# Performance work log

Measured on AMD Instinct MI355X. Metric: run time of the kernel, lower is better.

## Reference

```python
import jax, jax.numpy as jnp
import numpy as np

N_NODES = 50000
N_EDGES = 800000
N_FEAT = 128
HIDDEN = 128
N_CLASSES = 10
N_GRAPHS = 100


def setup_inputs() -> dict:
    key = jax.random.key(0)
    ks = jax.random.split(key, 16)
    x = jax.random.normal(ks[0], (N_NODES, N_FEAT), dtype=jnp.float32)
    edge_index = jax.random.randint(ks[1], (2, N_EDGES), 0, N_NODES, dtype=jnp.int64)
    batch = jnp.sort(jax.random.randint(ks[2], (N_NODES,), 0, N_GRAPHS, dtype=jnp.int64))

    def glorot(k, fi, fo):
        s = jnp.sqrt(6.0 / (fi + fo)).astype(jnp.float32)
        return jax.random.uniform(k, (fi, fo), jnp.float32, -s, s)

    return {
        "x": x,
        "edge_index": edge_index,
        "batch": batch,
        "W1": glorot(ks[3], N_FEAT, HIDDEN),
        "b1": jnp.zeros((HIDDEN,), jnp.float32),
        "W2": glorot(ks[4], HIDDEN, HIDDEN),
        "b2": jnp.zeros((HIDDEN,), jnp.float32),
        "W3": glorot(ks[5], HIDDEN, HIDDEN // 2),
        "b3": jnp.zeros((HIDDEN // 2,), jnp.float32),
        "Wf1": glorot(ks[6], HIDDEN // 2, 32),
        "bf1": jnp.zeros((32,), jnp.float32),
        "Wf2": glorot(ks[7], 32, N_CLASSES),
        "bf2": jnp.zeros((N_CLASSES,), jnp.float32),
    }


def _gcn_conv(x, row, col, norm, W, b, n_nodes):
    # GCNConv: x' = D^{-1/2}(A+I)D^{-1/2} (x W) + b
    h = x @ W                                            # [N, out]
    msg = h[row] * norm[:, None]                         # gather + scale per edge
    out = jax.ops.segment_sum(msg, col, num_segments=n_nodes)  # scatter-add to targets
    return out + b


def reference(x, edge_index, batch, W1, b1, W2, b2, W3, b3, Wf1, bf1, Wf2, bf2):
    n = x.shape[0]
    # add self-loops (PyG GCNConv default)
    loop = jnp.arange(n, dtype=edge_index.dtype)
    row = jnp.concatenate([edge_index[0], loop])
    col = jnp.concatenate([edge_index[1], loop])
    # symmetric normalization from in-degree at targets (edge_weight = 1)
    deg = jax.ops.segment_sum(jnp.ones_like(col, x.dtype), col, num_segments=n)
    dinv = jnp.where(deg > 0, jax.lax.rsqrt(deg), 0.0)
    norm = dinv[row] * dinv[col]                         # [E + N]

    h = jax.nn.relu(_gcn_conv(x, row, col, norm, W1, b1, n))
    h = jax.nn.relu(_gcn_conv(h, row, col, norm, W2, b2, n))
    h = jax.nn.relu(_gcn_conv(h, row, col, norm, W3, b3, n))

    # global_mean_pool over graphs
    sums = jax.ops.segment_sum(h, batch, num_segments=N_GRAPHS)
    cnts = jax.ops.segment_sum(jnp.ones((n,), h.dtype), batch, num_segments=N_GRAPHS)
    pooled = sums / jnp.maximum(cnts, 1.0)[:, None]      # [G, hidden//2]

    h = jax.nn.relu(pooled @ Wf1 + bf1)
    logits = h @ Wf2 + bf2                               # [G, num_classes]
    return logits
```

## Files before the change

kernel.cpp:

```cpp
#include <hip/hip_runtime.h>
#include <hip/hip_fp16.h>


#define NGRAPH 100
#define CAP 64

typedef _Float16 f16x8 __attribute__((ext_vector_type(8)));
typedef float f32x4 __attribute__((ext_vector_type(4)));
typedef float fx2 __attribute__((ext_vector_type(2)));


__global__ __launch_bounds__(256) void prep_all(const float* __restrict__ W1,
                                                const float* __restrict__ W2,
                                                const float* __restrict__ W3,
                                                __half* __restrict__ Wt1,
                                                __half* __restrict__ Wt2,
                                                __half* __restrict__ Wt3,
                                                int* __restrict__ cnt,
                                                float* __restrict__ pooled, int n) {
    const int idx = blockIdx.x * 256 + threadIdx.x;
    if (idx < 16384) {
        int nn = idx >> 7, k = idx & 127;
        Wt1[idx] = __float2half(W1[k * 128 + nn]);
    } else if (idx < 32768) {
        int j = idx - 16384;
        int nn = j >> 7, k = j & 127;
        Wt2[j] = __float2half(W2[k * 128 + nn]);
    } else if (idx < 40960) {
        int j = idx - 32768;
        int nn = j >> 7, k = j & 127;
        Wt3[j] = __float2half(W3[k * 64 + nn]);
    }
    if (idx < n) cnt[idx] = 0;
    if (idx < NGRAPH * 64) pooled[idx] = 0.0f;
}


__global__ void fill_bucket(const int* __restrict__ row, const int* __restrict__ col,
                            int* __restrict__ cnt, int* __restrict__ bucket,
                            int E, int colsPerGroup) {
    const int g  = blockIdx.x & 7;
    const int gb = blockIdx.x >> 3;
    const int nb = gridDim.x >> 3;
    const int lo = g * colsPerGroup, hi = lo + colsPerGroup;
    for (int e = gb * 256 + threadIdx.x; e < E; e += nb * 256) {
        int c = col[e];
        if (c >= lo && c < hi) {
            int pos = atomicAdd(&cnt[c], 1);
            bucket[c * CAP + pos] = row[e];
        }
    }
}


template <int OUT, bool F16IN>
__global__ __launch_bounds__(256) void gemm_mfma(const void* __restrict__ Xv,
                                                 const __half* __restrict__ Wt,
                                                 const float* __restrict__ bias_in,
                                                 const int* __restrict__ cnt,
                                                 __half* __restrict__ Yh, int n) {
    __shared__ _Float16 Xs[64 * 128];
    __shared__ _Float16 Ws[OUT * 128];
    __shared__ float bs[128];

    const float*  Xf = (const float*)Xv;
    const __half* Xh = (const __half*)Xv;

    const int t = threadIdx.x;
    if (t < 128) bs[t] = (bias_in != nullptr) ? bias_in[t] : 0.0f;
    __syncthreads();

    const int row0 = blockIdx.x * 64;
    const bool do_relu = (bias_in != nullptr);

    for (int c = t; c < 64 * 16; c += 256) {
        const int r = c >> 4, q = c & 15;
        const int gr = row0 + r;
        float vals[8];
        #pragma unroll
        for (int i = 0; i < 8; ++i) vals[i] = 0.0f;
        if (gr < n) {
            if (F16IN) {
                f16x8 hv = *(const f16x8*)&Xh[(size_t)gr * 128 + q * 8];
                #pragma unroll
                for (int i = 0; i < 8; ++i) vals[i] = (float)hv[i];
            } else {
                float4 va = *(const float4*)&Xf[(size_t)gr * 128 + q * 8];
                float4 vb = *(const float4*)&Xf[(size_t)gr * 128 + q * 8 + 4];
                vals[0] = va.x; vals[1] = va.y; vals[2] = va.z; vals[3] = va.w;
                vals[4] = vb.x; vals[5] = vb.y; vals[6] = vb.z; vals[7] = vb.w;
            }
        }
        if (do_relu) {
            const int k = q * 8;
            #pragma unroll
            for (int i = 0; i < 8; ++i) vals[i] = fmaxf(vals[i] + bs[k + i], 0.f);
        }
        f16x8 hv;
        #pragma unroll
        for (int i = 0; i < 8; ++i) hv[i] = (_Float16)vals[i];
        *(f16x8*)&Xs[(size_t)((r << 4) + (q ^ (r & 15))) * 8] = hv;
    }
    for (int c = t; c < OUT * 16; c += 256) {
        const int nn = c >> 4, q = c & 15;
        f16x8 w = *(const f16x8*)&Wt[nn * 128 + q * 8];
        *(f16x8*)&Ws[(size_t)((nn << 4) + (q ^ (nn & 15))) * 8] = w;
    }
    __syncthreads();

    constexpr int NT = OUT / 16;
    const int lane = t & 63, wave = t >> 6;
    const int m = lane & 15, quad = lane >> 4;

    f32x4 acc[NT];
    #pragma unroll
    for (int i = 0; i < NT; ++i) acc[i] = (f32x4){0.f, 0.f, 0.f, 0.f};

    #pragma unroll
    for (int s = 0; s < 4; ++s) {
        const int qa = s * 4 + quad;
        f16x8 a = *(const f16x8*)&Xs[(size_t)(((wave * 16 + m) << 4) + (qa ^ m)) * 8];
        #pragma unroll
        for (int tt = 0; tt < NT; ++tt) {
            f16x8 b = *(const f16x8*)&Ws[(size_t)(((tt * 16 + m) << 4) + (qa ^ m)) * 8];
            acc[tt] = __builtin_amdgcn_mfma_f32_16x16x32_f16(a, b, acc[tt], 0, 0, 0);
        }
    }

    #pragma unroll
    for (int i = 0; i < 4; ++i) {
        const int gr = row0 + wave * 16 + quad * 4 + i;
        if (gr < n) {
            const float dw = 1.0f / sqrtf((float)(cnt[gr] + 1));
            #pragma unroll
            for (int tt = 0; tt < NT; ++tt)
                Yh[(size_t)gr * OUT + tt * 16 + m] = __float2half(acc[tt][i] * dw);
        }
    }
}


template <int F>
__global__ void gather_kernel(const __half* __restrict__ hs, const int* __restrict__ cnt,
                              const int* __restrict__ bucket,
                              __half* __restrict__ outh, int n) {
    const int lane = threadIdx.x & 63;
    const int c = (blockIdx.x * blockDim.x + threadIdx.x) >> 6;
    if (c >= n) return;
    const int deg = cnt[c];
    const int beg = c * CAP;
    const int end = beg + deg;
    const int last = end - 1;
    const float w = 1.0f / sqrtf((float)(deg + 1));
    const float2* hq = (const float2*)hs;

    auto cvt = [](float2 raw) {
        __half2 ha = *(__half2*)&raw.x;
        __half2 hb = *(__half2*)&raw.y;
        float2 fa = __half22float2(ha);
        float2 fb = __half22float2(hb);
        return make_float4(fa.x, fa.y, fb.x, fb.y);
    };

    if (F == 128) {
        const int half = lane >> 5;
        const int l    = lane & 31;
        float4 acc = make_float4(0.f, 0.f, 0.f, 0.f);
        if (half == 0) acc = cvt(hq[(size_t)c * 32 + l]);
        const int chunks = (deg + 7) >> 3;
        int j = beg + half;
        for (int t = 0; t < chunks; ++t, j += 8) {
            const int j0 = j, j1 = j + 2, j2 = j + 4, j3 = j + 6;
            const int s0 = __builtin_nontemporal_load(&bucket[min(j0, last)]);
            const int s1 = __builtin_nontemporal_load(&bucket[min(j1, last)]);
            const int s2 = __builtin_nontemporal_load(&bucket[min(j2, last)]);
            const int s3 = __builtin_nontemporal_load(&bucket[min(j3, last)]);
            const float m0 = (j0 < end) ? 1.f : 0.f;
            const float m1 = (j1 < end) ? 1.f : 0.f;
            const float m2 = (j2 < end) ? 1.f : 0.f;
            const float m3 = (j3 < end) ? 1.f : 0.f;
            float4 v0 = cvt(hq[(size_t)s0 * 32 + l]);
            float4 v1 = cvt(hq[(size_t)s1 * 32 + l]);
            float4 v2 = cvt(hq[(size_t)s2 * 32 + l]);
            float4 v3 = cvt(hq[(size_t)s3 * 32 + l]);
            acc.x += m0 * v0.x + m1 * v1.x + m2 * v2.x + m3 * v3.x;
            acc.y += m0 * v0.y + m1 * v1.y + m2 * v2.y + m3 * v3.y;
            acc.z += m0 * v0.z + m1 * v1.z + m2 * v2.z + m3 * v3.z;
            acc.w += m0 * v0.w + m1 * v1.w + m2 * v2.w + m3 * v3.w;
        }
        acc.x += __shfl(acc.x, lane ^ 32);
        acc.y += __shfl(acc.y, lane ^ 32);
        acc.z += __shfl(acc.z, lane ^ 32);
        acc.w += __shfl(acc.w, lane ^ 32);
        if (half == 0) {
            __half2 h0 = __float22half2_rn(make_float2(w * acc.x, w * acc.y));
            __half2 h1 = __float22half2_rn(make_float2(w * acc.z, w * acc.w));
            fx2 o;
            o[0] = *(float*)&h0;
            o[1] = *(float*)&h1;
            __builtin_nontemporal_store(o, (fx2*)&outh[(size_t)c * 128 + l * 4]);
        }
    }
}


__global__ __launch_bounds__(256) void fused_gpool(const __half* __restrict__ hs,
                                                   const int* __restrict__ cnt,
                                                   const int* __restrict__ bucket,
                                                   const float* __restrict__ b3,
                                                   const int* __restrict__ batch,
                                                   float* __restrict__ pooled, int n) {
    const int lane  = threadIdx.x & 63;
    const int half  = lane >> 5;
    const int li    = lane & 31;
    const int wave  = (blockIdx.x * blockDim.x + threadIdx.x) >> 6;
    const int nwav  = (gridDim.x * blockDim.x) >> 6;
    const int chunk = (n + nwav - 1) / nwav;
    const int beg = wave * chunk;
    const int end = min(beg + chunk, n);
    if (beg >= end) return;
    const unsigned* h2 = (const unsigned*)hs;

    auto cvt2 = [](unsigned raw) { return __half22float2(*(__half2*)&raw); };

    const float bias0 = b3[li * 2], bias1 = b3[li * 2 + 1];
    int curg = batch[beg];
    float2 acc = make_float2(0.f, 0.f);
    for (int i = beg; i < end; ++i) {
        int g = batch[i];
        if (g != curg) {
            if (half == 0) {
                atomicAdd(&pooled[curg * 64 + li * 2],     acc.x);
                atomicAdd(&pooled[curg * 64 + li * 2 + 1], acc.y);
            }
            acc = make_float2(0.f, 0.f); curg = g;
        }
        const int deg = cnt[i];
        const float dv = 1.0f / sqrtf((float)(deg + 1));
        float2 sv = make_float2(0.f, 0.f);
        if (half == 0) sv = cvt2(h2[(size_t)i * 32 + li]);
        const int eb = i * CAP, ee = eb + deg;
        const int lastj = ee - 1;
        const int chks = (deg + 15) >> 4;
        int j = eb + half;
        for (int t = 0; t < chks; ++t, j += 16) {
            const int j0 = j,      j1 = j + 2,  j2 = j + 4,  j3 = j + 6;
            const int j4 = j + 8,  j5 = j + 10, j6 = j + 12, j7 = j + 14;
            const int a0 = __builtin_nontemporal_load(&bucket[min(j0, lastj)]);
            const int a1 = __builtin_nontemporal_load(&bucket[min(j1, lastj)]);
            const int a2 = __builtin_nontemporal_load(&bucket[min(j2, lastj)]);
            const int a3 = __builtin_nontemporal_load(&bucket[min(j3, lastj)]);
            const int a4 = __builtin_nontemporal_load(&bucket[min(j4, lastj)]);
            const int a5 = __builtin_nontemporal_load(&bucket[min(j5, lastj)]);
            const int a6 = __builtin_nontemporal_load(&bucket[min(j6, lastj)]);
            const int a7 = __builtin_nontemporal_load(&bucket[min(j7, lastj)]);
            const float m0 = (j0 < ee) ? 1.f : 0.f;
            const float m1 = (j1 < ee) ? 1.f : 0.f;
            const float m2 = (j2 < ee) ? 1.f : 0.f;
            const float m3 = (j3 < ee) ? 1.f : 0.f;
            const float m4 = (j4 < ee) ? 1.f : 0.f;
            const float m5 = (j5 < ee) ? 1.f : 0.f;
            const float m6 = (j6 < ee) ? 1.f : 0.f;
            const float m7 = (j7 < ee) ? 1.f : 0.f;
            float2 v0 = cvt2(h2[(size_t)a0 * 32 + li]);
            float2 v1 = cvt2(h2[(size_t)a1 * 32 + li]);
            float2 v2 = cvt2(h2[(size_t)a2 * 32 + li]);
            float2 v3 = cvt2(h2[(size_t)a3 * 32 + li]);
            float2 v4 = cvt2(h2[(size_t)a4 * 32 + li]);
            float2 v5 = cvt2(h2[(size_t)a5 * 32 + li]);
            float2 v6 = cvt2(h2[(size_t)a6 * 32 + li]);
            float2 v7 = cvt2(h2[(size_t)a7 * 32 + li]);
            sv.x += m0 * v0.x + m1 * v1.x + m2 * v2.x + m3 * v3.x
                  + m4 * v4.x + m5 * v5.x + m6 * v6.x + m7 * v7.x;
            sv.y += m0 * v0.y + m1 * v1.y + m2 * v2.y + m3 * v3.y
                  + m4 * v4.y + m5 * v5.y + m6 * v6.y + m7 * v7.y;
        }
        sv.x += __shfl(sv.x, lane ^ 32);
        sv.y += __shfl(sv.y, lane ^ 32);
        acc.x += fmaxf(dv * sv.x + bias0, 0.f);
        acc.y += fmaxf(dv * sv.y + bias1, 0.f);
    }
    if (half == 0) {
        atomicAdd(&pooled[curg * 64 + li * 2],     acc.x);
        atomicAdd(&pooled[curg * 64 + li * 2 + 1], acc.y);
    }
}


__global__ __launch_bounds__(64) void mlp_kernel(const float* __restrict__ pooled,
                                                 const int* __restrict__ batch,
                                                 const float* __restrict__ Wf1,
                                                 const float* __restrict__ bf1,
                                                 const float* __restrict__ Wf2,
                                                 const float* __restrict__ bf2,
                                                 float* __restrict__ out, int n) {
    const int g = blockIdx.x;
    const int t = threadIdx.x;

    auto lb = [&](int v) {
        int lo = 0, hi = n;
        while (lo < hi) { int mid = (lo + hi) >> 1; if (batch[mid] < v) lo = mid + 1; else hi = mid; }
        return lo;
    };
    const int cnt = lb(g + 1) - lb(g);

    __shared__ float pm[64];
    __shared__ float hid[32];

    pm[t] = pooled[g * 64 + t] / (float)(cnt > 0 ? cnt : 1);
    __syncthreads();

    if (t < 32) {
        float a = bf1[t];
        #pragma unroll
        for (int k = 0; k < 64; ++k) a += pm[k] * Wf1[k * 32 + t];
        hid[t] = fmaxf(a, 0.f);
    }
    __syncthreads();

    if (t < 10) {
        float a = bf2[t];
        #pragma unroll
        for (int k = 0; k < 32; ++k) a += hid[k] * Wf2[k * 10 + t];
        out[g * 10 + t] = a;
    }
}


extern "C" void kernel_launch(void* const* d_in, const int* in_sizes, int n_in,
                              void* d_out, int out_size, void* d_ws, size_t ws_size,
                              hipStream_t stream) {
    const float* x     = (const float*)d_in[0];
    const int*   edge  = (const int*)  d_in[1];
    const int*   batch = (const int*)  d_in[2];
    const float* W1    = (const float*)d_in[3];
    const float* b1    = (const float*)d_in[4];
    const float* W2    = (const float*)d_in[5];
    const float* b2    = (const float*)d_in[6];
    const float* W3    = (const float*)d_in[7];
    const float* b3    = (const float*)d_in[8];
    const float* Wf1   = (const float*)d_in[9];
    const float* bf1   = (const float*)d_in[10];
    const float* Wf2   = (const float*)d_in[11];
    const float* bf2   = (const float*)d_in[12];
    float* out = (float*)d_out;

    const int E = in_sizes[1] / 2;
    const int n = in_sizes[2];
    const int* row = edge;
    const int* col = edge + E;

    const int colsPerGroup = (n + 7) / 8;

    const size_t n_pad = ((size_t)n + 64) & ~(size_t)63;
    char* wsb = (char*)d_ws;
    int*    cnt    = (int*)wsb;                  wsb += n_pad * 4;
    float*  pooled = (float*)wsb;                wsb += NGRAPH * 64 * 4;
    int*    bucket = (int*)wsb;                  wsb += (size_t)n_pad * CAP * 4;
    __half* Wt1    = (__half*)wsb;               wsb += 16384 * 2;
    __half* Wt2    = (__half*)wsb;               wsb += 16384 * 2;
    __half* Wt3    = (__half*)wsb;               wsb += 8192 * 2;
    __half* bufA   = (__half*)wsb;               wsb += (size_t)n * 128 * 2;
    __half* bufB   = (__half*)wsb;

    prep_all<<<256, 256, 0, stream>>>(W1, W2, W3, Wt1, Wt2, Wt3, cnt, pooled, n);
    fill_bucket<<<1024, 256, 0, stream>>>(row, col, cnt, bucket, E, colsPerGroup);

    const int ggemm = (n + 63) / 64;
    const int gath_grid = (n * 64 + 255) / 256;

    gemm_mfma<128, false><<<ggemm, 256, 0, stream>>>(x, Wt1, nullptr, cnt, bufA, n);
    gather_kernel<128><<<gath_grid, 256, 0, stream>>>(bufA, cnt, bucket, bufB, n);
    gemm_mfma<128, true><<<ggemm, 256, 0, stream>>>(bufB, Wt2, b1, cnt, bufA, n);
    gather_kernel<128><<<gath_grid, 256, 0, stream>>>(bufA, cnt, bucket, bufB, n);
    gemm_mfma<64, true><<<ggemm, 256, 0, stream>>>(bufB, Wt3, b2, cnt, bufA, n);
    fused_gpool<<<2048, 256, 0, stream>>>(bufA, cnt, bucket, b3, batch, pooled, n);
    mlp_kernel<<<NGRAPH, 64, 0, stream>>>(pooled, batch, Wf1, bf1, Wf2, bf2, out, n);
}
```

Before: 276.4 us.

## Drop LDS staging in MFMA GEMM and simplify edge bucketing to single pass

The GEMM kernel no longer stages X and W tiles through shared memory. Each lane now loads its A fragment and B weight fragments straight from global memory and feeds them to the MFMA, which removes the LDS writes, reads and barriers. The bucket fill drops the 8-way column-group partitioning, where every block re-scanned the whole edge list, and does one pass over the edges with a guard against overflowing the bucket capacity. The trade-off is uncached, repeated global loads of weights per wave, and more atomic contention spread across all columns at once. The capacity guard also makes bucket contents silently incomplete if a node's degree exceeds CAP, whereas before they overflowed.

```diff
diff --git a/kernel.cpp b/kernel.cpp
--- a/kernel.cpp
+++ b/kernel.cpp
@@ -37,18 +37,11 @@
 
 
 __global__ void fill_bucket(const int* __restrict__ row, const int* __restrict__ col,
-                            int* __restrict__ cnt, int* __restrict__ bucket,
-                            int E, int colsPerGroup) {
-    const int g  = blockIdx.x & 7;
-    const int gb = blockIdx.x >> 3;
-    const int nb = gridDim.x >> 3;
-    const int lo = g * colsPerGroup, hi = lo + colsPerGroup;
-    for (int e = gb * 256 + threadIdx.x; e < E; e += nb * 256) {
-        int c = col[e];
-        if (c >= lo && c < hi) {
-            int pos = atomicAdd(&cnt[c], 1);
-            bucket[c * CAP + pos] = row[e];
-        }
+                            int* __restrict__ cnt, int* __restrict__ bucket, int E) {
+    for (int e = blockIdx.x * 256 + threadIdx.x; e < E; e += gridDim.x * 256) {
+        const int c = col[e];
+        const int pos = atomicAdd(&cnt[c], 1);
+        if (pos < CAP) bucket[c * CAP + pos] = row[e];
     }
 }
 
@@ -59,82 +52,71 @@
                                                  const float* __restrict__ bias_in,
                                                  const int* __restrict__ cnt,
                                                  __half* __restrict__ Yh, int n) {
-    __shared__ _Float16 Xs[64 * 128];
-    __shared__ _Float16 Ws[OUT * 128];
-    __shared__ float bs[128];
+    const int t = threadIdx.x;
+    const int wave = t >> 6, lane = t & 63;
+    const int m = lane & 15, quad = lane >> 4;
+    const int row0 = blockIdx.x * 64 + wave * 16;
+    const int gr = row0 + m;
+    const bool do_relu = (bias_in != nullptr);
 
     const float*  Xf = (const float*)Xv;
     const __half* Xh = (const __half*)Xv;
 
-    const int t = threadIdx.x;
-    if (t < 128) bs[t] = (bias_in != nullptr) ? bias_in[t] : 0.0f;
-    __syncthreads();
-
-    const int row0 = blockIdx.x * 64;
-    const bool do_relu = (bias_in != nullptr);
-
-    for (int c = t; c < 64 * 16; c += 256) {
-        const int r = c >> 4, q = c & 15;
-        const int gr = row0 + r;
+    constexpr int NT = OUT / 16;
+    f32x4 acc[NT];
+    #pragma unroll
+    for (int i = 0; i < NT; ++i) acc[i] = (f32x4){0.f, 0.f, 0.f, 0.f};
+
+    #pragma unroll
+    for (int s = 0; s < 4; ++s) {
+        const int qa = s * 4 + quad;
+        const int k0 = qa * 8;
         float vals[8];
         #pragma unroll
         for (int i = 0; i < 8; ++i) vals[i] = 0.0f;
         if (gr < n) {
             if (F16IN) {
-                f16x8 hv = *(const f16x8*)&Xh[(size_t)gr * 128 + q * 8];
+                f16x8 hv = *(const f16x8*)&Xh[(size_t)gr * 128 + k0];
                 #pragma unroll
                 for (int i = 0; i < 8; ++i) vals[i] = (float)hv[i];
             } else {
-                float4 va = *(const float4*)&Xf[(size_t)gr * 128 + q * 8];
-                float4 vb = *(const float4*)&Xf[(size_t)gr * 128 + q * 8 + 4];
+                float4 va = *(const float4*)&Xf[(size_t)gr * 128 + k0];
+                float4 vb = *(const float4*)&Xf[(size_t)gr * 128 + k0 + 4];
                 vals[0] = va.x; vals[1] = va.y; vals[2] = va.z; vals[3] = va.w;
                 vals[4] = vb.x; vals[5] = vb.y; vals[6] = vb.z; vals[7] = vb.w;
             }
         }
         if (do_relu) {
-            const int k = q * 8;
-            #pragma unroll
-            for (int i = 0; i < 8; ++i) vals[i] = fmaxf(vals[i] + bs[k + i], 0.f);
-        }
-        f16x8 hv;
-        #pragma unroll
-        for (int i = 0; i < 8; ++i) hv[i] = (_Float16)vals[i];
-        *(f16x8*)&Xs[(size_t)((r << 4) + (q ^ (r & 15))) * 8] = hv;
-    }
-    for (int c = t; c < OUT * 16; c += 256) {
-        const int nn = c >> 4, q = c & 15;
-        f16x8 w = *(const f16x8*)&Wt[nn * 128 + q * 8];
-        *(f16x8*)&Ws[(size_t)((nn << 4) + (q ^ (nn & 15))) * 8] = w;
-    }
-    __syncthreads();
-
-    constexpr int NT = OUT / 16;
-    const int lane = t & 63, wave = t >> 6;
-    const int m = lane & 15, quad = lane >> 4;
-
-    f32x4 acc[NT];
-    #pragma unroll
-    for (int i = 0; i < NT; ++i) acc[i] = (f32x4){0.f, 0.f, 0.f, 0.f};
-
-    #pragma unroll
-    for (int s = 0; s < 4; ++s) {
-        const int qa = s * 4 + quad;
-        f16x8 a = *(const f16x8*)&Xs[(size_t)(((wave * 16 + m) << 4) + (qa ^ m)) * 8];
+            float4 b0 = *(const float4*)&bias_in[k0];
+            float4 b1 = *(const float4*)&bias_in[k0 + 4];
+            vals[0] = fmaxf(vals[0] + b0.x, 0.f);
+            vals[1] = fmaxf(vals[1] + b0.y, 0.f);
+            vals[2] = fmaxf(vals[2] + b0.z, 0.f);
+            vals[3] = fmaxf(vals[3] + b0.w, 0.f);
+            vals[4] = fmaxf(vals[4] + b1.x, 0.f);
+            vals[5] = fmaxf(vals[5] + b1.y, 0.f);
+            vals[6] = fmaxf(vals[6] + b1.z, 0.f);
+            vals[7] = fmaxf(vals[7] + b1.w, 0.f);
+        }
+        f16x8 a;
+        #pragma unroll
+        for (int i = 0; i < 8; ++i) a[i] = (_Float16)vals[i];
+
         #pragma unroll
         for (int tt = 0; tt < NT; ++tt) {
-            f16x8 b = *(const f16x8*)&Ws[(size_t)(((tt * 16 + m) << 4) + (qa ^ m)) * 8];
+            f16x8 b = *(const f16x8*)&Wt[(size_t)(tt * 16 + m) * 128 + k0];
             acc[tt] = __builtin_amdgcn_mfma_f32_16x16x32_f16(a, b, acc[tt], 0, 0, 0);
         }
     }
 
     #pragma unroll
     for (int i = 0; i < 4; ++i) {
-        const int gr = row0 + wave * 16 + quad * 4 + i;
-        if (gr < n) {
-            const float dw = 1.0f / sqrtf((float)(cnt[gr] + 1));
+        const int go = row0 + quad * 4 + i;
+        if (go < n) {
+            const float dw = 1.0f / sqrtf((float)(cnt[go] + 1));
             #pragma unroll
             for (int tt = 0; tt < NT; ++tt)
-                Yh[(size_t)gr * OUT + tt * 16 + m] = __float2half(acc[tt][i] * dw);
+                Yh[(size_t)go * OUT + tt * 16 + m] = __float2half(acc[tt][i] * dw);
         }
     }
 }
@@ -350,8 +332,6 @@
     const int* row = edge;
     const int* col = edge + E;
 
-    const int colsPerGroup = (n + 7) / 8;
-
     const size_t n_pad = ((size_t)n + 64) & ~(size_t)63;
     char* wsb = (char*)d_ws;
     int*    cnt    = (int*)wsb;                  wsb += n_pad * 4;
@@ -364,7 +344,7 @@
     __half* bufB   = (__half*)wsb;
 
     prep_all<<<256, 256, 0, stream>>>(W1, W2, W3, Wt1, Wt2, Wt3, cnt, pooled, n);
-    fill_bucket<<<1024, 256, 0, stream>>>(row, col, cnt, bucket, E, colsPerGroup);
+    fill_bucket<<<1024, 256, 0, stream>>>(row, col, cnt, bucket, E);
 
     const int ggemm = (n + 63) / 64;
     const int gath_grid = (n * 64 + 255) / 256;
```

Result: slower. 318.0 us (+15.1%).

## Fuse bucket fill with first GEMM and defer source-degree scaling to gather

Applied to the files above, without the earlier changes.

The edge bucketing and the first layer's X·W1 GEMM now run as one launch, with separate block ranges for each, so they can overlap. Degree counts are not final while the GEMM runs, so the GEMM output is left unscaled. The first gather then applies the source-node normalisation per edge by reading cnt[src], and the target scaling on the self-loop term. This removes a serial kernel boundary, at the cost of extra scattered cnt loads and rsqrt work in the first gather, and possible contention between atomic and MFMA blocks.

```diff
diff --git a/kernel.cpp b/kernel.cpp
--- a/kernel.cpp
+++ b/kernel.cpp
@@ -36,29 +36,12 @@
 }
 
 
-__global__ void fill_bucket(const int* __restrict__ row, const int* __restrict__ col,
-                            int* __restrict__ cnt, int* __restrict__ bucket,
-                            int E, int colsPerGroup) {
-    const int g  = blockIdx.x & 7;
-    const int gb = blockIdx.x >> 3;
-    const int nb = gridDim.x >> 3;
-    const int lo = g * colsPerGroup, hi = lo + colsPerGroup;
-    for (int e = gb * 256 + threadIdx.x; e < E; e += nb * 256) {
-        int c = col[e];
-        if (c >= lo && c < hi) {
-            int pos = atomicAdd(&cnt[c], 1);
-            bucket[c * CAP + pos] = row[e];
-        }
-    }
-}
-
-
-template <int OUT, bool F16IN>
-__global__ __launch_bounds__(256) void gemm_mfma(const void* __restrict__ Xv,
-                                                 const __half* __restrict__ Wt,
-                                                 const float* __restrict__ bias_in,
-                                                 const int* __restrict__ cnt,
-                                                 __half* __restrict__ Yh, int n) {
+template <int OUT, bool F16IN, bool SCALE>
+__device__ __forceinline__ void gemm_body(const int bid, const void* __restrict__ Xv,
+                                          const __half* __restrict__ Wt,
+                                          const float* __restrict__ bias_in,
+                                          const int* __restrict__ cnt,
+                                          __half* __restrict__ Yh, const int n) {
     __shared__ _Float16 Xs[64 * 128];
     __shared__ _Float16 Ws[OUT * 128];
     __shared__ float bs[128];
@@ -70,7 +53,7 @@
     if (t < 128) bs[t] = (bias_in != nullptr) ? bias_in[t] : 0.0f;
     __syncthreads();
 
-    const int row0 = blockIdx.x * 64;
+    const int row0 = bid * 64;
     const bool do_relu = (bias_in != nullptr);
 
     for (int c = t; c < 64 * 16; c += 256) {
@@ -131,7 +114,7 @@
     for (int i = 0; i < 4; ++i) {
         const int gr = row0 + wave * 16 + quad * 4 + i;
         if (gr < n) {
-            const float dw = 1.0f / sqrtf((float)(cnt[gr] + 1));
+            const float dw = SCALE ? (1.0f / sqrtf((float)(cnt[gr] + 1))) : 1.0f;
             #pragma unroll
             for (int tt = 0; tt < NT; ++tt)
                 Yh[(size_t)gr * OUT + tt * 16 + m] = __float2half(acc[tt][i] * dw);
@@ -139,8 +122,43 @@
     }
 }
 
-
-template <int F>
+template <int OUT, bool F16IN>
+__global__ __launch_bounds__(256) void gemm_mfma(const void* __restrict__ Xv,
+                                                 const __half* __restrict__ Wt,
+                                                 const float* __restrict__ bias_in,
+                                                 const int* __restrict__ cnt,
+                                                 __half* __restrict__ Yh, int n) {
+    gemm_body<OUT, F16IN, true>(blockIdx.x, Xv, Wt, bias_in, cnt, Yh, n);
+}
+
+
+__global__ __launch_bounds__(256) void fill_gemm1(const int* __restrict__ row,
+                                                  const int* __restrict__ col,
+                                                  int* __restrict__ cnt,
+                                                  int* __restrict__ bucket,
+                                                  int E, int colsPerGroup, int fillBlocks,
+                                                  const float* __restrict__ x,
+                                                  const __half* __restrict__ Wt1,
+                                                  __half* __restrict__ Yh, int n) {
+    if ((int)blockIdx.x < fillBlocks) {
+        const int g  = blockIdx.x & 7;
+        const int gb = blockIdx.x >> 3;
+        const int nb = fillBlocks >> 3;
+        const int lo = g * colsPerGroup, hi = lo + colsPerGroup;
+        for (int e = gb * 256 + threadIdx.x; e < E; e += nb * 256) {
+            int c = col[e];
+            if (c >= lo && c < hi) {
+                int pos = atomicAdd(&cnt[c], 1);
+                bucket[c * CAP + pos] = row[e];
+            }
+        }
+    } else {
+        gemm_body<128, false, false>(blockIdx.x - fillBlocks, x, Wt1, nullptr, cnt, Yh, n);
+    }
+}
+
+
+template <int F, bool PRENORM>
 __global__ void gather_kernel(const __half* __restrict__ hs, const int* __restrict__ cnt,
                               const int* __restrict__ bucket,
                               __half* __restrict__ outh, int n) {
@@ -166,7 +184,10 @@
         const int half = lane >> 5;
         const int l    = lane & 31;
         float4 acc = make_float4(0.f, 0.f, 0.f, 0.f);
-        if (half == 0) acc = cvt(hq[(size_t)c * 32 + l]);
+        if (half == 0) {
+            acc = cvt(hq[(size_t)c * 32 + l]);
+            if (!PRENORM) { acc.x *= w; acc.y *= w; acc.z *= w; acc.w *= w; }
+        }
         const int chunks = (deg + 7) >> 3;
         int j = beg + half;
         for (int t = 0; t < chunks; ++t, j += 8) {
@@ -175,18 +196,24 @@
             const int s1 = __builtin_nontemporal_load(&bucket[min(j1, last)]);
             const int s2 = __builtin_nontemporal_load(&bucket[min(j2, last)]);
             const int s3 = __builtin_nontemporal_load(&bucket[min(j3, last)]);
-            const float m0 = (j0 < end) ? 1.f : 0.f;
-            const float m1 = (j1 < end) ? 1.f : 0.f;
-            const float m2 = (j2 < end) ? 1.f : 0.f;
-            const float m3 = (j3 < end) ? 1.f : 0.f;
+            float d0 = (j0 < end) ? 1.f : 0.f;
+            float d1 = (j1 < end) ? 1.f : 0.f;
+            float d2 = (j2 < end) ? 1.f : 0.f;
+            float d3 = (j3 < end) ? 1.f : 0.f;
+            if (!PRENORM) {
+                d0 *= 1.0f / sqrtf((float)(cnt[s0] + 1));
+                d1 *= 1.0f / sqrtf((float)(cnt[s1] + 1));
+                d2 *= 1.0f / sqrtf((float)(cnt[s2] + 1));
+                d3 *= 1.0f / sqrtf((float)(cnt[s3] + 1));
+            }
             float4 v0 = cvt(hq[(size_t)s0 * 32 + l]);
             float4 v1 = cvt(hq[(size_t)s1 * 32 + l]);
             float4 v2 = cvt(hq[(size_t)s2 * 32 + l]);
             float4 v3 = cvt(hq[(size_t)s3 * 32 + l]);
-            acc.x += m0 * v0.x + m1 * v1.x + m2 * v2.x + m3 * v3.x;
-            acc.y += m0 * v0.y + m1 * v1.y + m2 * v2.y + m3 * v3.y;
-            acc.z += m0 * v0.z + m1 * v1.z + m2 * v2.z + m3 * v3.z;
-            acc.w += m0 * v0.w + m1 * v1.w + m2 * v2.w + m3 * v3.w;
+            acc.x += d0 * v0.x + d1 * v1.x + d2 * v2.x + d3 * v3.x;
+            acc.y += d0 * v0.y + d1 * v1.y + d2 * v2.y + d3 * v3.y;
+            acc.z += d0 * v0.z + d1 * v1.z + d2 * v2.z + d3 * v3.z;
+            acc.w += d0 * v0.w + d1 * v1.w + d2 * v2.w + d3 * v3.w;
         }
         acc.x += __shfl(acc.x, lane ^ 32);
         acc.y += __shfl(acc.y, lane ^ 32);
@@ -351,6 +378,7 @@
     const int* col = edge + E;
 
     const int colsPerGroup = (n + 7) / 8;
+    const int fillBlocks = 1024;
 
     const size_t n_pad = ((size_t)n + 64) & ~(size_t)63;
     char* wsb = (char*)d_ws;
@@ -363,16 +391,16 @@
     __half* bufA   = (__half*)wsb;               wsb += (size_t)n * 128 * 2;
     __half* bufB   = (__half*)wsb;
 
-    prep_all<<<256, 256, 0, stream>>>(W1, W2, W3, Wt1, Wt2, Wt3, cnt, pooled, n);
-    fill_bucket<<<1024, 256, 0, stream>>>(row, col, cnt, bucket, E, colsPerGroup);
-
     const int ggemm = (n + 63) / 64;
     const int gath_grid = (n * 64 + 255) / 256;
 
-    gemm_mfma<128, false><<<ggemm, 256, 0, stream>>>(x, Wt1, nullptr, cnt, bufA, n);
-    gather_kernel<128><<<gath_grid, 256, 0, stream>>>(bufA, cnt, bucket, bufB, n);
+    prep_all<<<256, 256, 0, stream>>>(W1, W2, W3, Wt1, Wt2, Wt3, cnt, pooled, n);
+    fill_gemm1<<<fillBlocks + ggemm, 256, 0, stream>>>(row, col, cnt, bucket, E,
+                                                       colsPerGroup, fillBlocks,
+                                                       x, Wt1, bufA, n);
+    gather_kernel<128, false><<<gath_grid, 256, 0, stream>>>(bufA, cnt, bucket, bufB, n);
     gemm_mfma<128, true><<<ggemm, 256, 0, stream>>>(bufB, Wt2, b1, cnt, bufA, n);
-    gather_kernel<128><<<gath_grid, 256, 0, stream>>>(bufA, cnt, bucket, bufB, n);
+    gather_kernel<128, true><<<gath_grid, 256, 0, stream>>>(bufA, cnt, bucket, bufB, n);
     gemm_mfma<64, true><<<ggemm, 256, 0, stream>>>(bufB, Wt3, b2, cnt, bufA, n);
     fused_gpool<<<2048, 256, 0, stream>>>(bufA, cnt, bucket, b3, batch, pooled, n);
     mlp_kernel<<<NGRAPH, 64, 0, stream>>>(pooled, batch, Wf1, bf1, Wf2, bf2, out, n);
```

Measured after the change: 287.1 us. 3.9% more time.
